# Performance work log

Hardware: AMD Instinct MI355X
Metric: run time of the kernel (lower is better)

The kernel has to match this reference:

```python
import jax, jax.numpy as jnp
import numpy as np

NUM_EMBEDDINGS = 1024
EMBEDDING_DIM = 64
COMMITMENT_COST = 0.25


def setup_inputs() -> dict:
    key = jax.random.key(0)
    k1, k2 = jax.random.split(key)
    inputs = jax.random.normal(k1, (64, 32, 32, EMBEDDING_DIM), dtype=jnp.float32)
    # torch init is uniform(-1/K, 1/K); scale accordingly
    weight = jax.random.uniform(
        k2, (NUM_EMBEDDINGS, EMBEDDING_DIM), dtype=jnp.float32,
        minval=-1.0 / NUM_EMBEDDINGS, maxval=1.0 / NUM_EMBEDDINGS)
    return {"inputs": inputs, "weight": weight}


def reference(inputs, weight):
    input_shape = inputs.shape
    flat = inputs.reshape(-1, EMBEDDING_DIM)               # [N, D]
    distances = (jnp.sum(flat ** 2, axis=1, keepdims=True)
                 + jnp.sum(weight ** 2, axis=1)
                 - 2.0 * flat @ weight.T)                   # [N, K]
    encoding_indices = jnp.argmin(distances, axis=1)        # [N]
    # gather codes (equivalent to one-hot @ weight, but as a direct gather)
    quantized = weight[encoding_indices].reshape(input_shape)

    e_latent_loss = jnp.mean((jax.lax.stop_gradient(quantized) - inputs) ** 2)
    q_latent_loss = jnp.mean((quantized - jax.lax.stop_gradient(inputs)) ** 2)
    loss = q_latent_loss + COMMITMENT_COST * e_latent_loss

    # straight-through estimator
    quantized_ste = inputs + jax.lax.stop_gradient(quantized - inputs)

    # perplexity (equivalent to mean over the one-hot encodings)
    n_tokens = flat.shape[0]
    counts = jax.ops.segment_sum(
        jnp.ones((n_tokens,), jnp.float32), encoding_indices,
        num_segments=NUM_EMBEDDINGS)
    avg_probs = counts / n_tokens
    perplexity = jnp.exp(-jnp.sum(avg_probs * jnp.log(avg_probs + 1e-10)))

    indices_for_transformer = encoding_indices.reshape(input_shape[0], -1)
    return (loss, quantized_ste, perplexity, indices_for_transformer)
```

## Files before the change

kernel.cpp:

```cpp
#include <hip/hip_runtime.h>
#include <cstdint>
#include <cstddef>

#define N_TOKENS 65536
#define DIM 64
#define K_CODES 1024
#define NTH 256
#define NTHM 512
#define TPB 64
#define NCH 16

#define OFF_Q 1
#define OFF_PERP 4194305
#define OFF_IDX 4194306

#define MARGIN 1.5e-4f
#define HMARGIN 7.5e-5f

#define WS_LOSS   0
#define WS_FCNT   8
#define WS_COUNTS 16
#define WS_WHI    4112
#define WS_WLO    135184
#define WS_S2     266256
#define WS_FLIST  270352
#define WS_FBBEST 401424

typedef __attribute__((ext_vector_type(8))) short  s16x8;
typedef __attribute__((ext_vector_type(4))) float  f32x4;

__device__ __forceinline__ float fmulr(float a, float b){ return __fmul_rn(a,b); }
__device__ __forceinline__ float faddr(float a, float b){ return __fadd_rn(a,b); }

__device__ __forceinline__ unsigned short f2bf(float f) {
    unsigned u = __float_as_uint(f);
    unsigned r = u + 0x7fffu + ((u >> 16) & 1u);
    return (unsigned short)(r >> 16);
}
__device__ __forceinline__ float bf2f(unsigned short h) {
    return __uint_as_float(((unsigned)h) << 16);
}

__device__ float sumsq64_np(const float* __restrict__ p) {
    float s[16];
    #pragma unroll
    for (int l = 0; l < 16; ++l) {
        float a0 = fmulr(p[l],      p[l]);
        float a1 = fmulr(p[l + 16], p[l + 16]);
        float a2 = fmulr(p[l + 32], p[l + 32]);
        float a3 = fmulr(p[l + 48], p[l + 48]);
        s[l] = faddr(faddr(a0, a1), faddr(a2, a3));
    }
    #pragma unroll
    for (int len = 8; len >= 1; len >>= 1)
        #pragma unroll
        for (int l = 0; l < len; ++l)
            s[l] = faddr(s[l], s[l + len]);
    return s[0];
}

__device__ __forceinline__ void async_copy16(const void* g, void* l) {
    __builtin_amdgcn_global_load_lds(
        (const __attribute__((address_space(1))) void*)g,
        (__attribute__((address_space(3))) void*)l, 16, 0, 0);
}

__global__ void vq_prep(const float* __restrict__ W, unsigned short* __restrict__ Whi,
                        unsigned short* __restrict__ Wlo, float* __restrict__ s2g,
                        int* __restrict__ counts, int* __restrict__ gfcount,
                        double* __restrict__ loss_acc,
                        unsigned long long* __restrict__ fbbest) {
    int gid = blockIdx.x * NTH + threadIdx.x;
    for (int e = gid; e < K_CODES * DIM; e += 16384) {
        float x = W[e];
        unsigned short hi = f2bf(x);
        unsigned short lo = f2bf(__fsub_rn(x, bf2f(hi)));
        int j = e >> 6, k = e & 63;
        int pos = j * 64 + (((k >> 3) ^ (j & 7)) << 3) + (k & 7);
        Whi[pos] = hi; Wlo[pos] = lo;
    }
    #pragma unroll
    for (int i = 0; i < 4; ++i) fbbest[gid + 16384 * i] = ~0ULL;
    if (gid < K_CODES) { s2g[gid] = sumsq64_np(W + gid * 64); counts[gid] = 0; }
    if (gid == 0) { *loss_acc = 0.0; *gfcount = 0; }
}

__global__ __launch_bounds__(NTHM, 4)
void vq_main(const float* __restrict__ X, const float* __restrict__ W,
             const unsigned short* __restrict__ WhiG, const unsigned short* __restrict__ WloG,
             const float* __restrict__ s2g, float* __restrict__ out,
             double* __restrict__ loss_acc, int* __restrict__ counts,
             int* __restrict__ gfcount, unsigned short* __restrict__ gflist) {
    __shared__ __align__(16) char uraw[32768];
    __shared__ __align__(16) float s2s[K_CODES];
    __shared__ int fidx[TPB];
    __shared__ int flist[TPB];
    __shared__ int fcount, gbaseS;
    __shared__ double lred[8];

    unsigned short* xs_hi = (unsigned short*)uraw;
    unsigned short* xs_lo = (unsigned short*)(uraw + 16384);
    float (*sm1)[TPB] = (float(*)[TPB])uraw;
    float (*sm2)[TPB] = (float(*)[TPB])(uraw + 1024);
    int   (*si1)[TPB] = (int  (*)[TPB])(uraw + 2048);

    const int tid  = threadIdx.x;
    const int lane = tid & 63, wave = tid >> 6;
    const int quad = lane >> 4, lrow = lane & 15;
    const int tg   = wave & 1;
    const int chd  = wave >> 1;
    const int t0   = blockIdx.x * TPB;

    if (tid == 0) fcount = 0;

    if (tid < 256) *(f32x4*)&s2s[tid * 4] = *(const f32x4*)&s2g[tid * 4];
    {
        int t = tid >> 3, kb = tid & 7;
        const float* src = X + (size_t)(t0 + t) * DIM + kb * 8;
        float v[8];
        *(f32x4*)v       = *(const f32x4*)src;
        *(f32x4*)(v + 4) = *(const f32x4*)(src + 4);
        unsigned short h[8], l[8];
        #pragma unroll
        for (int k = 0; k < 8; ++k) {
            h[k] = f2bf(v[k]);
            l[k] = f2bf(__fsub_rn(v[k], bf2f(h[k])));
        }
        int base = t * 64 + ((kb ^ (t & 7)) << 3);
        *(s16x8*)&xs_hi[base] = *(s16x8*)h;
        *(s16x8*)&xs_lo[base] = *(s16x8*)l;
    }
    __syncthreads();

    s16x8 a_h0[2], a_h1[2], a_l0[2], a_l1[2];
    #pragma unroll
    for (int rt = 0; rt < 2; ++rt) {
        int tf = tg * 32 + rt * 16 + lrow;
        int sA = tf & 7;
        a_h0[rt] = *(const s16x8*)&xs_hi[tf * 64 + (((0 + quad) ^ sA) << 3)];
        a_h1[rt] = *(const s16x8*)&xs_hi[tf * 64 + (((4 + quad) ^ sA) << 3)];
        a_l0[rt] = *(const s16x8*)&xs_lo[tf * 64 + (((0 + quad) ^ sA) << 3)];
        a_l1[rt] = *(const s16x8*)&xs_lo[tf * 64 + (((4 + quad) ^ sA) << 3)];
    }
    __syncthreads();

    {
        const char* gh = (const char*)WhiG;
        const char* gl = (const char*)WloG;
        char* b0 = uraw + wave * 1024;
        char* b1 = uraw + 16384 + wave * 1024;
        async_copy16(gh + tid * 16,        b0);
        async_copy16(gl + tid * 16,        b0 + 8192);
        async_copy16(gh + 8192 + tid * 16, b1);
        async_copy16(gl + 8192 + tid * 16, b1 + 8192);
    }

    float m1v[8], m2v[8]; int m1i[8];
    #pragma unroll
    for (int ri = 0; ri < 8; ++ri) { m1v[ri] = -3.4e38f; m2v[ri] = -3.4e38f; m1i[ri] = 0x7fffffff; }

    for (int ch = 0; ch < NCH; ++ch) {
        if (ch < NCH - 1) asm volatile("s_waitcnt vmcnt(2)" ::: "memory");
        else              asm volatile("s_waitcnt vmcnt(0)" ::: "memory");
        __builtin_amdgcn_s_barrier();
        __builtin_amdgcn_sched_barrier(0);

        const unsigned short* wh = (const unsigned short*)(uraw + (ch & 1) * 16384);
        const unsigned short* wl = wh + 4096;
        {
            int lc = chd * 16 + lrow;
            int sB = lrow & 7;
            const unsigned short* bh = &wh[lc * 64];
            const unsigned short* bl = &wl[lc * 64];
            s16x8 b_h0 = *(const s16x8*)&bh[((0 + quad) ^ sB) << 3];
            s16x8 b_h1 = *(const s16x8*)&bh[((4 + quad) ^ sB) << 3];
            s16x8 b_l0 = *(const s16x8*)&bl[((0 + quad) ^ sB) << 3];
            s16x8 b_l1 = *(const s16x8*)&bl[((4 + quad) ^ sB) << 3];
            int jcode = ch * 64 + lc;
            float s2v = s2s[jcode];
            float ainit = fmulr(-0.5f, s2v);
            #pragma unroll
            for (int rt = 0; rt < 2; ++rt) {
                f32x4 acc = {ainit, ainit, ainit, ainit};
                acc = __builtin_amdgcn_mfma_f32_16x16x32_bf16(a_h0[rt], b_h0, acc, 0, 0, 0);
                acc = __builtin_amdgcn_mfma_f32_16x16x32_bf16(a_h1[rt], b_h1, acc, 0, 0, 0);
                acc = __builtin_amdgcn_mfma_f32_16x16x32_bf16(a_h0[rt], b_l0, acc, 0, 0, 0);
                acc = __builtin_amdgcn_mfma_f32_16x16x32_bf16(a_h1[rt], b_l1, acc, 0, 0, 0);
                acc = __builtin_amdgcn_mfma_f32_16x16x32_bf16(a_l0[rt], b_h0, acc, 0, 0, 0);
                acc = __builtin_amdgcn_mfma_f32_16x16x32_bf16(a_l1[rt], b_h1, acc, 0, 0, 0);
                #pragma unroll
                for (int r = 0; r < 4; ++r) {
                    float a = acc[r];
                    int ri = rt * 4 + r;
                    bool gt = a > m1v[ri];
                    float sec = gt ? m1v[ri] : a;
                    m2v[ri] = fmaxf(m2v[ri], sec);
                    m1v[ri] = gt ? a : m1v[ri];
                    m1i[ri] = gt ? jcode : m1i[ri];
                }
            }
        }

        __builtin_amdgcn_sched_barrier(0);
        __builtin_amdgcn_s_barrier();
        __builtin_amdgcn_sched_barrier(0);
        if (ch + 2 < NCH) {
            const char* gh = (const char*)WhiG + (ch + 2) * 8192;
            const char* gl = (const char*)WloG + (ch + 2) * 8192;
            char* lb = uraw + (ch & 1) * 16384 + wave * 1024;
            async_copy16(gh + tid * 16, lb);
            async_copy16(gl + tid * 16, lb + 8192);
        }
    }

    #pragma unroll
    for (int m = 1; m <= 8; m <<= 1) {
        #pragma unroll
        for (int ri = 0; ri < 8; ++ri) {
            float o1v = __shfl_xor(m1v[ri], m, 64);
            int   o1i = __shfl_xor(m1i[ri], m, 64);
            float o2v = __shfl_xor(m2v[ri], m, 64);
            bool take = (o1v > m1v[ri]) || (o1v == m1v[ri] && o1i < m1i[ri]);
            float loser = take ? m1v[ri] : o1v;
            m2v[ri] = fmaxf(fmaxf(m2v[ri], o2v), loser);
            if (take) { m1v[ri] = o1v; m1i[ri] = o1i; }
        }
    }
    if (lrow == 0) {
        #pragma unroll
        for (int ri = 0; ri < 8; ++ri) {
            int rt = ri >> 2, r = ri & 3;
            int t = tg * 32 + rt * 16 + quad * 4 + r;
            sm1[chd][t] = m1v[ri];
            sm2[chd][t] = m2v[ri];
            si1[chd][t] = m1i[ri];
        }
    }
    __syncthreads();
    if (tid < TPB) {
        int t = tid;
        float w1 = sm1[0][t], w2 = sm2[0][t];
        int   wi = si1[0][t];
        #pragma unroll
        for (int h = 1; h < 4; ++h) {
            float c1 = sm1[h][t]; int ci = si1[h][t];
            bool take = (c1 > w1) || (c1 == w1 && ci < wi);
            float loser = take ? w1 : c1;
            if (take) { w1 = c1; wi = ci; }
            w2 = fmaxf(fmaxf(w2, sm2[h][t]), loser);
        }
        bool fb = __fsub_rn(w1, w2) < HMARGIN;
        fidx[t] = fb ? (wi | (int)0x80000000) : wi;
        if (fb) { int p = atomicAdd(&fcount, 1); flist[p] = t; }
    }
    __syncthreads();

    double lsum = 0.0;
    #pragma unroll
    for (int i = 0; i < 2; ++i) {
        int e4 = tid + NTHM * i;
        int t = e4 >> 4, d4 = (e4 & 15) * 4;
        int iv = fidx[t];
        if (iv >= 0) {
            f32x4 q = *(const f32x4*)&W[iv * 64 + d4];
            f32x4 x = *(const f32x4*)&X[(size_t)(t0 + t) * 64 + d4];
            *(f32x4*)&out[(size_t)OFF_Q + (size_t)(t0 + t) * 64 + d4] = q;
            #pragma unroll
            for (int c = 0; c < 4; ++c) {
                float df = __fsub_rn(q[c], x[c]);
                lsum += (double)fmulr(df, df);
            }
        }
    }
    #pragma unroll
    for (int off = 32; off >= 1; off >>= 1) lsum += __shfl_down(lsum, off, 64);
    if (lane == 0) lred[wave] = lsum;
    if (tid < TPB) {
        int iv = fidx[tid];
        if (iv >= 0) {
            atomicAdd(&counts[iv], 1);
            out[(size_t)OFF_IDX + t0 + tid] = (float)iv;
        }
    }
    if (tid == 0) gbaseS = atomicAdd(gfcount, fcount);
    __syncthreads();
    if (tid < fcount) gflist[gbaseS + tid] = (unsigned short)(t0 + flist[tid]);
    if (tid == 0)
        atomicAdd(loss_acc, lred[0] + lred[1] + lred[2] + lred[3] +
                            lred[4] + lred[5] + lred[6] + lred[7]);
}

__global__ __launch_bounds__(NTH, 3)
void vq_fb_scan(const float* __restrict__ X, const float* __restrict__ W,
                const float* __restrict__ s2g, const int* __restrict__ gfcount,
                const unsigned short* __restrict__ gflist,
                unsigned long long* __restrict__ fbbest) {
    int count = *gfcount;
    if (count <= 0) return;
    int nunits = ((count + 63) >> 6) << 3;

    __shared__ __align__(16) float xsf[64 * 64];
    __shared__ __align__(16) float wsf[128 * 64];
    __shared__ float s1f[64];

    const int tid = threadIdx.x;
    const int r = tid & 15, c = tid >> 4;

    for (int u = blockIdx.x; u < nunits; u += 1024) {
        int bt = u >> 3, bc = u & 7;
        int base = bt << 6;
        int nt = min(64, count - base);
        __syncthreads();

        #pragma unroll
        for (int i = 0; i < 4; ++i) {
            int idx = tid + NTH * i;
            int t = idx >> 4, kb = idx & 15;
            int tok = gflist[base + (t < nt ? t : 0)];
            f32x4 v = *(const f32x4*)(X + (size_t)tok * 64 + kb * 4);
            *(f32x4*)&xsf[t * 64 + ((kb ^ ((t >> 2) & 7)) << 2)] = v;
        }
        #pragma unroll
        for (int i = 0; i < 8; ++i) {
            int idx = tid + NTH * i;
            int jl = idx >> 4, kb = idx & 15;
            f32x4 v = *(const f32x4*)(W + (size_t)(bc * 128 + jl) * 64 + kb * 4);
            *(f32x4*)&wsf[jl * 64 + ((kb ^ ((jl >> 3) & 7)) << 2)] = v;
        }
        if (tid < nt) s1f[tid] = sumsq64_np(X + (size_t)gflist[base + tid] * 64);
        __syncthreads();

        float acc[4][8];
        #pragma unroll
        for (int i = 0; i < 4; ++i)
            #pragma unroll
            for (int m = 0; m < 8; ++m) acc[i][m] = 0.0f;

        #pragma unroll
        for (int kb = 0; kb < 16; ++kb) {
            f32x4 xv[4], wv[8];
            #pragma unroll
            for (int i = 0; i < 4; ++i)
                xv[i] = *(const f32x4*)&xsf[(4 * r + i) * 64 + ((kb ^ (r & 7)) << 2)];
            #pragma unroll
            for (int m = 0; m < 8; ++m)
                wv[m] = *(const f32x4*)&wsf[(8 * c + m) * 64 + ((kb ^ (c & 7)) << 2)];
            #pragma unroll
            for (int i = 0; i < 4; ++i)
                #pragma unroll
                for (int m = 0; m < 8; ++m) {
                    acc[i][m] = __builtin_fmaf(xv[i][0], wv[m][0], acc[i][m]);
                    acc[i][m] = __builtin_fmaf(xv[i][1], wv[m][1], acc[i][m]);
                    acc[i][m] = __builtin_fmaf(xv[i][2], wv[m][2], acc[i][m]);
                    acc[i][m] = __builtin_fmaf(xv[i][3], wv[m][3], acc[i][m]);
                }
        }
        float runVal[4]; int runIdx[4];
        #pragma unroll
        for (int i = 0; i < 4; ++i) { runVal[i] = 3.4e38f; runIdx[i] = 0; }
        #pragma unroll
        for (int i = 0; i < 4; ++i) {
            float s1v = s1f[4 * r + i];
            #pragma unroll
            for (int m = 0; m < 8; ++m) {
                int jl = 8 * c + m;
                float d = faddr(faddr(s1v, s2g[bc * 128 + jl]), fmulr(-2.0f, acc[i][m]));
                if (d < runVal[i]) { runVal[i] = d; runIdx[i] = bc * 128 + jl; }
            }
        }

        __syncthreads();
        unsigned long long* red = (unsigned long long*)wsf;
        #pragma unroll
        for (int i = 0; i < 4; ++i) {
            unsigned long long pk =
                ((unsigned long long)__float_as_uint(runVal[i]) << 32) |
                (unsigned long long)(unsigned int)runIdx[i];
            red[(4 * r + i) * 16 + c] = pk;
        }
        __syncthreads();
        if (tid < nt) {
            unsigned long long best = red[tid * 16];
            #pragma unroll
            for (int cc = 1; cc < 16; ++cc) {
                unsigned long long v = red[tid * 16 + cc];
                best = (v < best) ? v : best;
            }
            atomicMin(&fbbest[base + tid], best);
        }
    }
}

__global__ __launch_bounds__(NTH, 4)
void vq_fb_fin(const float* __restrict__ X, const float* __restrict__ W,
               const int* __restrict__ gfcount, const unsigned short* __restrict__ gflist,
               const unsigned long long* __restrict__ fbbest, float* __restrict__ out,
               double* __restrict__ loss_acc, int* __restrict__ counts) {
    int count = *gfcount;
    __shared__ double lred[4];
    const int tid = threadIdx.x;
    const int lane = tid & 63, wave = tid >> 6;
    double lsum = 0.0;
    int total = count << 4;
    for (int g = blockIdx.x * NTH + tid; g < total; g += NTH * 256) {
        int p = g >> 4, d4 = (g & 15) << 2;
        int tok = gflist[p];
        int idx = (int)(fbbest[p] & 0xffffffffULL);
        f32x4 q = *(const f32x4*)&W[idx * 64 + d4];
        f32x4 x = *(const f32x4*)&X[(size_t)tok * 64 + d4];
        *(f32x4*)&out[(size_t)OFF_Q + (size_t)tok * 64 + d4] = q;
        #pragma unroll
        for (int cc = 0; cc < 4; ++cc) {
            float df = __fsub_rn(q[cc], x[cc]);
            lsum += (double)fmulr(df, df);
        }
        if ((g & 15) == 0) {
            out[(size_t)OFF_IDX + tok] = (float)idx;
            atomicAdd(&counts[idx], 1);
        }
    }
    #pragma unroll
    for (int off = 32; off >= 1; off >>= 1) lsum += __shfl_down(lsum, off, 64);
    if (lane == 0) lred[wave] = lsum;
    __syncthreads();
    if (tid == 0) {
        double t = lred[0] + lred[1] + lred[2] + lred[3];
        if (t != 0.0) atomicAdd(loss_acc, t);
    }
}

__global__ void vq_final(const int* __restrict__ counts,
                         const double* __restrict__ loss_acc,
                         float* __restrict__ out) {
    __shared__ double hred[4];
    int tid = threadIdx.x;
    double h = 0.0;
    for (int j = tid; j < K_CODES; j += 256) {
        double p = (double)counts[j] / 65536.0;
        h += p * log(p + 1e-10);
    }
    #pragma unroll
    for (int off = 32; off >= 1; off >>= 1) h += __shfl_down(h, off, 64);
    if ((tid & 63) == 0) hred[tid >> 6] = h;
    __syncthreads();
    if (tid == 0) {
        double H = hred[0] + hred[1] + hred[2] + hred[3];
        out[OFF_PERP] = (float)exp(-H);
        double ls = *loss_acc;
        float Lf = (float)(ls / 4194304.0);
        out[0] = faddr(Lf, fmulr(0.25f, Lf));
    }
}

extern "C" void kernel_launch(void* const* d_in, const int* in_sizes, int n_in,
                              void* d_out, int out_size, void* d_ws, size_t ws_size,
                              hipStream_t stream) {
    const float* X = (const float*)d_in[0];
    const float* W = (const float*)d_in[1];
    float* out = (float*)d_out;
    char* ws = (char*)d_ws;
    double* loss_acc = (double*)(ws + WS_LOSS);
    int* gfcount = (int*)(ws + WS_FCNT);
    int* counts = (int*)(ws + WS_COUNTS);
    unsigned short* Whi = (unsigned short*)(ws + WS_WHI);
    unsigned short* Wlo = (unsigned short*)(ws + WS_WLO);
    float* s2g = (float*)(ws + WS_S2);
    unsigned short* gflist = (unsigned short*)(ws + WS_FLIST);
    unsigned long long* fbbest = (unsigned long long*)(ws + WS_FBBEST);

    vq_prep<<<64, NTH, 0, stream>>>(W, Whi, Wlo, s2g, counts, gfcount, loss_acc, fbbest);
    vq_main<<<N_TOKENS / TPB, NTHM, 0, stream>>>(X, W, Whi, Wlo, s2g, out,
                                                 loss_acc, counts, gfcount, gflist);
    vq_fb_scan<<<1024, NTH, 0, stream>>>(X, W, s2g, gfcount, gflist, fbbest);
    vq_fb_fin<<<256, NTH, 0, stream>>>(X, W, gfcount, gflist, fbbest, out,
                                       loss_acc, counts);
    vq_final<<<1, NTH, 0, stream>>>(counts, loss_acc, out);
}
```

Measured before the change: 170.8 us.

## Double tokens per block, fuse fallback scan/finish/final kernels via completion counters

The main kernel now handles 128 tokens per block with 4 token-groups of waves, so each loaded codebook chunk is reused across twice as many tokens. Each wave covers two 16-code sub-tiles per chunk, and the cross-wave merge shrinks from four to two candidates. The top-2 tracking uses a v_med3 instruction in place of a select/max sequence. The fallback fin and final kernels are folded into the scan kernel using per-tile and global done counters with threadfences, which removes two launches but adds atomic and last-block synchronisation logic. The prep kernel is also reworked to one element per thread over 256 blocks.

```diff
diff --git a/kernel.cpp b/kernel.cpp
--- a/kernel.cpp
+++ b/kernel.cpp
@@ -7,7 +7,7 @@
 #define K_CODES 1024
 #define NTH 256
 #define NTHM 512
-#define TPB 64
+#define TPB 128
 #define NCH 16
 
 #define OFF_Q 1
@@ -25,6 +25,7 @@
 #define WS_S2     266256
 #define WS_FLIST  270352
 #define WS_FBBEST 401424
+#define WS_DONE   925712
 
 typedef __attribute__((ext_vector_type(8))) short  s16x8;
 typedef __attribute__((ext_vector_type(4))) float  f32x4;
@@ -69,18 +70,19 @@
                         unsigned short* __restrict__ Wlo, float* __restrict__ s2g,
                         int* __restrict__ counts, int* __restrict__ gfcount,
                         double* __restrict__ loss_acc,
-                        unsigned long long* __restrict__ fbbest) {
+                        unsigned long long* __restrict__ fbbest,
+                        int* __restrict__ done) {
     int gid = blockIdx.x * NTH + threadIdx.x;
-    for (int e = gid; e < K_CODES * DIM; e += 16384) {
-        float x = W[e];
+    {
+        float x = W[gid];
         unsigned short hi = f2bf(x);
         unsigned short lo = f2bf(__fsub_rn(x, bf2f(hi)));
-        int j = e >> 6, k = e & 63;
+        int j = gid >> 6, k = gid & 63;
         int pos = j * 64 + (((k >> 3) ^ (j & 7)) << 3) + (k & 7);
         Whi[pos] = hi; Wlo[pos] = lo;
     }
-    #pragma unroll
-    for (int i = 0; i < 4; ++i) fbbest[gid + 16384 * i] = ~0ULL;
+    fbbest[gid] = ~0ULL;
+    if (gid < 1025) done[gid] = 0;
     if (gid < K_CODES) { s2g[gid] = sumsq64_np(W + gid * 64); counts[gid] = 0; }
     if (gid == 0) { *loss_acc = 0.0; *gfcount = 0; }
 }
@@ -107,15 +109,17 @@
     const int tid  = threadIdx.x;
     const int lane = tid & 63, wave = tid >> 6;
     const int quad = lane >> 4, lrow = lane & 15;
-    const int tg   = wave & 1;
-    const int chd  = wave >> 1;
+    const int tg   = wave & 3;
+    const int chd  = wave >> 2;
     const int t0   = blockIdx.x * TPB;
 
     if (tid == 0) fcount = 0;
 
     if (tid < 256) *(f32x4*)&s2s[tid * 4] = *(const f32x4*)&s2g[tid * 4];
-    {
-        int t = tid >> 3, kb = tid & 7;
+    #pragma unroll
+    for (int i = 0; i < 2; ++i) {
+        int g = tid + NTHM * i;
+        int t = g >> 3, kb = g & 7;
         const float* src = X + (size_t)(t0 + t) * DIM + kb * 8;
         float v[8];
         *(f32x4*)v       = *(const f32x4*)src;
@@ -167,8 +171,9 @@
 
         const unsigned short* wh = (const unsigned short*)(uraw + (ch & 1) * 16384);
         const unsigned short* wl = wh + 4096;
-        {
-            int lc = chd * 16 + lrow;
+        #pragma unroll
+        for (int ct2 = 0; ct2 < 2; ++ct2) {
+            int lc = chd * 32 + ct2 * 16 + lrow;
             int sB = lrow & 7;
             const unsigned short* bh = &wh[lc * 64];
             const unsigned short* bl = &wl[lc * 64];
@@ -192,10 +197,10 @@
                 for (int r = 0; r < 4; ++r) {
                     float a = acc[r];
                     int ri = rt * 4 + r;
+                    asm("v_med3_f32 %0, %1, %2, %3"
+                        : "=v"(m2v[ri]) : "v"(a), "v"(m1v[ri]), "v"(m2v[ri]));
                     bool gt = a > m1v[ri];
-                    float sec = gt ? m1v[ri] : a;
-                    m2v[ri] = fmaxf(m2v[ri], sec);
-                    m1v[ri] = gt ? a : m1v[ri];
+                    m1v[ri] = fmaxf(m1v[ri], a);
                     m1i[ri] = gt ? jcode : m1i[ri];
                 }
             }
@@ -239,16 +244,14 @@
     __syncthreads();
     if (tid < TPB) {
         int t = tid;
-        float w1 = sm1[0][t], w2 = sm2[0][t];
-        int   wi = si1[0][t];
-        #pragma unroll
-        for (int h = 1; h < 4; ++h) {
-            float c1 = sm1[h][t]; int ci = si1[h][t];
-            bool take = (c1 > w1) || (c1 == w1 && ci < wi);
-            float loser = take ? w1 : c1;
-            if (take) { w1 = c1; wi = ci; }
-            w2 = fmaxf(fmaxf(w2, sm2[h][t]), loser);
-        }
+        float a1 = sm1[0][t], b1 = sm1[1][t];
+        int   ia = si1[0][t], ib = si1[1][t];
+        float a2 = sm2[0][t], b2 = sm2[1][t];
+        bool take = (b1 > a1) || (b1 == a1 && ib < ia);
+        float w1 = take ? b1 : a1;
+        int   wi = take ? ib : ia;
+        float loser = take ? a1 : b1;
+        float w2 = fmaxf(fmaxf(a2, b2), loser);
         bool fb = __fsub_rn(w1, w2) < HMARGIN;
         fidx[t] = fb ? (wi | (int)0x80000000) : wi;
         if (fb) { int p = atomicAdd(&fcount, 1); flist[p] = t; }
@@ -257,7 +260,7 @@
 
     double lsum = 0.0;
     #pragma unroll
-    for (int i = 0; i < 2; ++i) {
+    for (int i = 0; i < 4; ++i) {
         int e4 = tid + NTHM * i;
         int t = e4 >> 4, d4 = (e4 & 15) * 4;
         int iv = fidx[t];
@@ -290,20 +293,51 @@
                             lred[4] + lred[5] + lred[6] + lred[7]);
 }
 
+__device__ void final_scalars(int* counts, double* loss_acc, float* out,
+                              int tid, double* hred) {
+    double h = 0.0;
+    for (int j = tid; j < K_CODES; j += NTH) {
+        int cj = atomicAdd(&counts[j], 0);
+        double p = (double)cj / 65536.0;
+        h += p * log(p + 1e-10);
+    }
+    #pragma unroll
+    for (int off = 32; off >= 1; off >>= 1) h += __shfl_down(h, off, 64);
+    if ((tid & 63) == 0) hred[tid >> 6] = h;
+    __syncthreads();
+    if (tid == 0) {
+        double H = hred[0] + hred[1] + hred[2] + hred[3];
+        out[OFF_PERP] = (float)exp(-H);
+        double ls = atomicAdd(loss_acc, 0.0);
+        float Lf = (float)(ls / 4194304.0);
+        out[0] = faddr(Lf, fmulr(0.25f, Lf));
+    }
+}
+
 __global__ __launch_bounds__(NTH, 3)
-void vq_fb_scan(const float* __restrict__ X, const float* __restrict__ W,
-                const float* __restrict__ s2g, const int* __restrict__ gfcount,
-                const unsigned short* __restrict__ gflist,
-                unsigned long long* __restrict__ fbbest) {
+void vq_fb(const float* __restrict__ X, const float* __restrict__ W,
+           const float* __restrict__ s2g, const int* __restrict__ gfcount,
+           const unsigned short* __restrict__ gflist,
+           unsigned long long* __restrict__ fbbest, int* __restrict__ done,
+           float* __restrict__ out, double* __restrict__ loss_acc,
+           int* __restrict__ counts) {
     int count = *gfcount;
-    if (count <= 0) return;
-    int nunits = ((count + 63) >> 6) << 3;
+    const int tid = threadIdx.x;
+    __shared__ double lredf[4];
+    if (count <= 0) {
+        if (blockIdx.x == 0) final_scalars(counts, loss_acc, out, tid, lredf);
+        return;
+    }
+    int nbt = (count + 63) >> 6;
+    int nunits = nbt << 3;
 
     __shared__ __align__(16) float xsf[64 * 64];
     __shared__ __align__(16) float wsf[128 * 64];
     __shared__ float s1f[64];
-
-    const int tid = threadIdx.x;
+    __shared__ int gidx[64];
+    __shared__ int lastflag;
+
+    const int lane = tid & 63, wave = tid >> 6;
     const int r = tid & 15, c = tid >> 4;
 
     for (int u = blockIdx.x; u < nunits; u += 1024) {
@@ -388,67 +422,55 @@
             }
             atomicMin(&fbbest[base + tid], best);
         }
-    }
-}
-
-__global__ __launch_bounds__(NTH, 4)
-void vq_fb_fin(const float* __restrict__ X, const float* __restrict__ W,
-               const int* __restrict__ gfcount, const unsigned short* __restrict__ gflist,
-               const unsigned long long* __restrict__ fbbest, float* __restrict__ out,
-               double* __restrict__ loss_acc, int* __restrict__ counts) {
-    int count = *gfcount;
-    __shared__ double lred[4];
-    const int tid = threadIdx.x;
-    const int lane = tid & 63, wave = tid >> 6;
-    double lsum = 0.0;
-    int total = count << 4;
-    for (int g = blockIdx.x * NTH + tid; g < total; g += NTH * 256) {
-        int p = g >> 4, d4 = (g & 15) << 2;
-        int tok = gflist[p];
-        int idx = (int)(fbbest[p] & 0xffffffffULL);
-        f32x4 q = *(const f32x4*)&W[idx * 64 + d4];
-        f32x4 x = *(const f32x4*)&X[(size_t)tok * 64 + d4];
-        *(f32x4*)&out[(size_t)OFF_Q + (size_t)tok * 64 + d4] = q;
-        #pragma unroll
-        for (int cc = 0; cc < 4; ++cc) {
-            float df = __fsub_rn(q[cc], x[cc]);
-            lsum += (double)fmulr(df, df);
-        }
-        if ((g & 15) == 0) {
-            out[(size_t)OFF_IDX + tok] = (float)idx;
-            atomicAdd(&counts[idx], 1);
-        }
-    }
-    #pragma unroll
-    for (int off = 32; off >= 1; off >>= 1) lsum += __shfl_down(lsum, off, 64);
-    if (lane == 0) lred[wave] = lsum;
-    __syncthreads();
-    if (tid == 0) {
-        double t = lred[0] + lred[1] + lred[2] + lred[3];
-        if (t != 0.0) atomicAdd(loss_acc, t);
-    }
-}
-
-__global__ void vq_final(const int* __restrict__ counts,
-                         const double* __restrict__ loss_acc,
-                         float* __restrict__ out) {
-    __shared__ double hred[4];
-    int tid = threadIdx.x;
-    double h = 0.0;
-    for (int j = tid; j < K_CODES; j += 256) {
-        double p = (double)counts[j] / 65536.0;
-        h += p * log(p + 1e-10);
-    }
-    #pragma unroll
-    for (int off = 32; off >= 1; off >>= 1) h += __shfl_down(h, off, 64);
-    if ((tid & 63) == 0) hred[tid >> 6] = h;
-    __syncthreads();
-    if (tid == 0) {
-        double H = hred[0] + hred[1] + hred[2] + hred[3];
-        out[OFF_PERP] = (float)exp(-H);
-        double ls = *loss_acc;
-        float Lf = (float)(ls / 4194304.0);
-        out[0] = faddr(Lf, fmulr(0.25f, Lf));
+        __threadfence();
+        __syncthreads();
+        if (tid == 0) lastflag = (atomicAdd(&done[bt], 1) == 7);
+        __syncthreads();
+        if (lastflag) {
+            if (tid < 64) {
+                int idx = -1;
+                if (tid < nt) {
+                    unsigned long long b = atomicMax(&fbbest[base + tid], 0ULL);
+                    idx = (int)(b & 0xffffffffu);
+                    int tok = gflist[base + tid];
+                    out[(size_t)OFF_IDX + tok] = (float)idx;
+                    atomicAdd(&counts[idx], 1);
+                }
+                gidx[tid] = idx;
+            }
+            __syncthreads();
+            double lsum = 0.0;
+            #pragma unroll
+            for (int i = 0; i < 4; ++i) {
+                int e4 = tid + NTH * i;
+                int t = e4 >> 4, d4 = (e4 & 15) * 4;
+                if (t < nt) {
+                    int tok = gflist[base + t];
+                    int idx = gidx[t];
+                    f32x4 q = *(const f32x4*)&W[idx * 64 + d4];
+                    f32x4 x = *(const f32x4*)&X[(size_t)tok * 64 + d4];
+                    *(f32x4*)&out[(size_t)OFF_Q + (size_t)tok * 64 + d4] = q;
+                    #pragma unroll
+                    for (int cc = 0; cc < 4; ++cc) {
+                        float df = __fsub_rn(q[cc], x[cc]);
+                        lsum += (double)fmulr(df, df);
+                    }
+                }
+            }
+            #pragma unroll
+            for (int off = 32; off >= 1; off >>= 1) lsum += __shfl_down(lsum, off, 64);
+            if (lane == 0) lredf[wave] = lsum;
+            __syncthreads();
+            if (tid == 0) {
+                double s = lredf[0] + lredf[1] + lredf[2] + lredf[3];
+                if (s != 0.0) atomicAdd(loss_acc, s);
+            }
+            __threadfence();
+            __syncthreads();
+            if (tid == 0) lastflag = (atomicAdd(&done[1024], 1) == nbt - 1);
+            __syncthreads();
+            if (lastflag) final_scalars(counts, loss_acc, out, tid, lredf);
+        }
     }
 }
 
@@ -467,12 +489,12 @@
     float* s2g = (float*)(ws + WS_S2);
     unsigned short* gflist = (unsigned short*)(ws + WS_FLIST);
     unsigned long long* fbbest = (unsigned long long*)(ws + WS_FBBEST);
-
-    vq_prep<<<64, NTH, 0, stream>>>(W, Whi, Wlo, s2g, counts, gfcount, loss_acc, fbbest);
+    int* done = (int*)(ws + WS_DONE);
+
+    vq_prep<<<256, NTH, 0, stream>>>(W, Whi, Wlo, s2g, counts, gfcount, loss_acc,
+                                     fbbest, done);
     vq_main<<<N_TOKENS / TPB, NTHM, 0, stream>>>(X, W, Whi, Wlo, s2g, out,
                                                  loss_acc, counts, gfcount, gflist);
-    vq_fb_scan<<<1024, NTH, 0, stream>>>(X, W, s2g, gfcount, gflist, fbbest);
-    vq_fb_fin<<<256, NTH, 0, stream>>>(X, W, gfcount, gflist, fbbest, out,
-                                       loss_acc, counts);
-    vq_final<<<1, NTH, 0, stream>>>(counts, loss_acc, out);
-}
+    vq_fb<<<1024, NTH, 0, stream>>>(X, W, s2g, gfcount, gflist, fbbest, done,
+                                    out, loss_acc, counts);
+}
```

Result: slower. 231.5 us (+35.5%).
